# Performance work log

Hardware: AMD Instinct MI355X
Metric: run time of the kernel (lower is better)

Reference implementation:

```python
import jax, jax.numpy as jnp
import numpy as np

LN_EPS = 1e-5  # torch LayerNorm default


def setup_inputs() -> dict:
    key = jax.random.key(0)
    k1, k2, k3 = jax.random.split(key, 3)
    B, L, D = 8, 2048, 1024
    CS, CD = 8192, 16
    x = jax.random.normal(k1, (B, L, D), dtype=jnp.float32)
    # xavier_uniform for Linear(dim, codebook_dim): bound = sqrt(6/(fan_in+fan_out))
    bound = float(np.sqrt(6.0 / (D + CD)))
    W = jax.random.uniform(k2, (CD, D), dtype=jnp.float32, minval=-bound, maxval=bound)
    codebook = jax.random.normal(k3, (CS, CD), dtype=jnp.float32)
    return {"x": x, "W": W, "codebook": codebook}


def reference(x, W, codebook):
    # random projection: (B,L,D) @ (D,CD) -> (B,L,CD)
    z = jnp.einsum("bld,cd->blc", x, W)
    # LayerNorm over last dim, no affine
    mu = jnp.mean(z, axis=-1, keepdims=True)
    var = jnp.mean(jnp.square(z - mu), axis=-1, keepdims=True)
    z = (z - mu) / jnp.sqrt(var + LN_EPS)
    # squared euclidean distance via matmul decomposition (avoids (B,L,CS,CD) tensor):
    # ||z - c||^2 = ||z||^2 - 2 z.c + ||c||^2 ; argmin is identical to argmin of the norm
    z_sq = jnp.sum(jnp.square(z), axis=-1, keepdims=True)        # (B,L,1)
    c_sq = jnp.sum(jnp.square(codebook), axis=-1)                # (CS,)
    d2 = z_sq - 2.0 * jnp.einsum("blc,kc->blk", z, codebook) + c_sq  # (B,L,CS)
    codes = jnp.argmin(d2, axis=-1)                              # (B,L) int32
    return codes
```

## Files before the change

kernel.cpp:

```cpp
#include <hip/hip_runtime.h>
#include <math.h>

#define D      1024
#define CD     16
#define CS     8192
#define ROWS   16384
#define LN_EPS 1e-5f
#define KCHUNK 512
#define NCHUNK (CS / KCHUNK)
#define CPAD   56

typedef __attribute__((ext_vector_type(8))) short short8;
typedef __attribute__((ext_vector_type(4))) float f32x4;

__device__ inline unsigned short bf16_rne(float v) {
    unsigned u = __float_as_uint(v);
    unsigned r = u + 0x7FFFu + ((u >> 16) & 1u);
    return (unsigned short)(r >> 16);
}
__device__ inline short8 ld8(const unsigned short* p) { return *(const short8*)p; }

__device__ inline void split3(float v, unsigned short& a, unsigned short& b, unsigned short& c) {
    unsigned u = __float_as_uint(v);
    unsigned r = u + 0x7FFFu + ((u >> 16) & 1u);
    a = (unsigned short)(r >> 16);
    float r1 = v - __uint_as_float(r & 0xFFFF0000u);
    unsigned u1 = __float_as_uint(r1);
    unsigned r1b = u1 + 0x7FFFu + ((u1 >> 16) & 1u);
    b = (unsigned short)(r1b >> 16);
    float r2 = r1 - __uint_as_float(r1b & 0xFFFF0000u);
    c = bf16_rne(r2);
}

__global__ __launch_bounds__(256) void pack_all(const float* __restrict__ W,
                                                const float* __restrict__ cb,
                                                unsigned short* __restrict__ wb,
                                                unsigned short* __restrict__ cbp,
                                                float* __restrict__ nhc)
{
    const int t = threadIdx.x;
    if (blockIdx.x < 32) {
        int k = blockIdx.x * 256 + t;
        const float* c = cb + (long)k * CD;
        unsigned short* o = cbp + (long)k * 48;
        float csq = 0.f;
        #pragma unroll
        for (int d = 0; d < 16; ++d) {
            float v = c[d];
            csq = fmaf(v, v, csq);
            unsigned short h0, h1, h2;
            split3(v, h0, h1, h2);
            o[d] = h0; o[16 + d] = h1; o[32 + d] = h2;
        }
        nhc[k] = -0.5f * csq;
    } else {
        int tid = (blockIdx.x - 32) * 256 + t;
        int gk   = tid / 192;
        int rem  = tid % 192;
        int term = rem >> 6;
        int L    = rem & 63;
        int n = L & 15, q = L >> 4;
        const float* src = W + n * D + gk * 32 + q * 8;
        unsigned short* dst = wb + (size_t)tid * 8;
        #pragma unroll
        for (int j = 0; j < 8; ++j) {
            unsigned short h0, h1, h2;
            split3(src[j], h0, h1, h2);
            dst[j] = term == 0 ? h0 : (term == 1 ? h1 : h2);
        }
    }
}

__global__ __launch_bounds__(256, 4) void proj_ln(const float* __restrict__ x,
                                                  const unsigned short* __restrict__ wb,
                                                  unsigned short* __restrict__ zp)
{
    __shared__ float part[3][64][4];
    const int t = threadIdx.x;
    const int L = t & 63;
    const int kq = t >> 6;
    const int rt = blockIdx.x;
    const int n = L & 15, q = L >> 4;

    const float* xrow = x + (size_t)(rt * 16 + n) * D + kq * 256 + q * 8;
    const unsigned short* wbase = wb + (size_t)(kq * 8) * 1536;

    f32x4 acc0 = {0.f, 0.f, 0.f, 0.f};
    f32x4 acc1 = {0.f, 0.f, 0.f, 0.f};
    #pragma unroll
    for (int kk = 0; kk < 8; ++kk) {
        float4 xa = *(const float4*)(xrow + kk * 32);
        float4 xb = *(const float4*)(xrow + kk * 32 + 4);
        const unsigned short* wp = wbase + (size_t)kk * 1536 + L * 8;
        short8 w0 = ld8(wp);
        short8 w1 = ld8(wp + 512);
        short8 w2 = ld8(wp + 1024);
        float vs[8] = {xa.x, xa.y, xa.z, xa.w, xb.x, xb.y, xb.z, xb.w};
        short8 x0, x1, x2;
        #pragma unroll
        for (int j = 0; j < 8; ++j) {
            unsigned short h0, h1, h2;
            split3(vs[j], h0, h1, h2);
            x0[j] = (short)h0; x1[j] = (short)h1; x2[j] = (short)h2;
        }
        acc0 = __builtin_amdgcn_mfma_f32_16x16x32_bf16(x0, w0, acc0, 0, 0, 0);
        acc1 = __builtin_amdgcn_mfma_f32_16x16x32_bf16(x0, w1, acc1, 0, 0, 0);
        acc0 = __builtin_amdgcn_mfma_f32_16x16x32_bf16(x1, w0, acc0, 0, 0, 0);
        acc1 = __builtin_amdgcn_mfma_f32_16x16x32_bf16(x1, w1, acc1, 0, 0, 0);
        acc0 = __builtin_amdgcn_mfma_f32_16x16x32_bf16(x0, w2, acc0, 0, 0, 0);
        acc1 = __builtin_amdgcn_mfma_f32_16x16x32_bf16(x2, w0, acc1, 0, 0, 0);
    }

    if (kq != 0) {
        #pragma unroll
        for (int r = 0; r < 4; ++r) part[kq - 1][L][r] = acc0[r] + acc1[r];
    }
    __syncthreads();
    if (kq == 0) {
        #pragma unroll
        for (int r = 0; r < 4; ++r) {
            float zv = acc0[r] + acc1[r] + part[0][L][r] + part[1][L][r] + part[2][L][r];
            float s = zv;
            for (int m = 1; m < 16; m <<= 1) s += __shfl_xor(s, m, 64);
            float mu = s * (1.f / 16.f);
            float dd = zv - mu;
            float v2 = dd * dd;
            for (int m = 1; m < 16; m <<= 1) v2 += __shfl_xor(v2, m, 64);
            float var = v2 * (1.f / 16.f);
            float zn = dd / sqrtf(var + LN_EPS);
            unsigned short h0, h1, h2;
            split3(zn, h0, h1, h2);
            unsigned short* zr = zp + (size_t)(rt * 16 + q * 4 + r) * 48;
            zr[n] = h0; zr[16 + n] = h1; zr[32 + n] = h2;
        }
    }
}

__global__ __launch_bounds__(256, 2) void dist_argmin(const unsigned short* __restrict__ zp,
                                                      const unsigned short* __restrict__ cbp,
                                                      const float* __restrict__ nhc,
                                                      float* __restrict__ pbest,
                                                      int* __restrict__ pidx)
{
    __shared__ __align__(16) unsigned short cl[KCHUNK * CPAD];
    __shared__ float ql[KCHUNK];
    const int t = threadIdx.x;
    const int kbase = blockIdx.y * KCHUNK;

    {
        const float4* src = (const float4*)(cbp + (size_t)kbase * 48);
        #pragma unroll
        for (int i = 0; i < 12; ++i) {
            int idx = t + i * 256;
            int k = idx / 6, c = idx % 6;
            *(float4*)(cl + (size_t)k * CPAD + c * 8) = src[idx];
        }
        if (t < KCHUNK / 4) ((float4*)ql)[t] = ((const float4*)(nhc + kbase))[t];
    }
    __syncthreads();

    const int L = t & 63;
    const int w = t >> 6;
    const int n = L & 15;
    const int q = L >> 4;

    const int oa2 = (q * 8 + 16) & 31;
    const int oa3 = q < 2 ? 32 + q * 8 : (q - 2) * 8;
    const int ob3 = q < 2 ? q * 8 : 16 + q * 8;

    short8 a1[4], a2[4], a3[4];
    const int rt0 = blockIdx.x * 16 + w * 4;
    #pragma unroll
    for (int j = 0; j < 4; ++j) {
        const unsigned short* zr = zp + (size_t)((rt0 + j) * 16 + n) * 48;
        a1[j] = ld8(zr + q * 8);
        a2[j] = ld8(zr + oa2);
        a3[j] = ld8(zr + oa3);
    }

    float best[4][4];
    int   bi[4][4];
    #pragma unroll
    for (int j = 0; j < 4; ++j)
        #pragma unroll
        for (int r = 0; r < 4; ++r) { best[j][r] = -INFINITY; bi[j][r] = 0; }

    #pragma unroll 2
    for (int tt = 0; tt < KCHUNK / 16; ++tt) {
        const unsigned short* cb_t = cl + (size_t)(tt * 16 + n) * CPAD;
        short8 b1 = ld8(cb_t + q * 8);
        short8 b3 = ld8(cb_t + ob3);
        float bneg = ql[tt * 16 + n];
        f32x4 bias = {bneg, bneg, bneg, bneg};
        int code = kbase + tt * 16 + n;
        f32x4 acc[4];
        #pragma unroll
        for (int j = 0; j < 4; ++j)
            acc[j] = __builtin_amdgcn_mfma_f32_16x16x32_bf16(a1[j], b1, bias, 0, 0, 0);
        #pragma unroll
        for (int j = 0; j < 4; ++j)
            acc[j] = __builtin_amdgcn_mfma_f32_16x16x32_bf16(a2[j], b1, acc[j], 0, 0, 0);
        #pragma unroll
        for (int j = 0; j < 4; ++j)
            acc[j] = __builtin_amdgcn_mfma_f32_16x16x32_bf16(a3[j], b3, acc[j], 0, 0, 0);
        #pragma unroll
        for (int j = 0; j < 4; ++j)
            #pragma unroll
            for (int r = 0; r < 4; ++r)
                if (acc[j][r] > best[j][r]) { best[j][r] = acc[j][r]; bi[j][r] = code; }
    }

    #pragma unroll
    for (int mask = 1; mask < 16; mask <<= 1) {
        #pragma unroll
        for (int j = 0; j < 4; ++j)
            #pragma unroll
            for (int r = 0; r < 4; ++r) {
                float s2 = __shfl_xor(best[j][r], mask, 64);
                int   i2 = __shfl_xor(bi[j][r], mask, 64);
                if (s2 > best[j][r] || (s2 == best[j][r] && i2 < bi[j][r])) {
                    best[j][r] = s2; bi[j][r] = i2;
                }
            }
    }
    if (n == 0) {
        #pragma unroll
        for (int j = 0; j < 4; ++j)
            #pragma unroll
            for (int r = 0; r < 4; ++r) {
                int row = (rt0 + j) * 16 + q * 4 + r;
                pbest[(size_t)row * NCHUNK + blockIdx.y] = best[j][r];
                pidx [(size_t)row * NCHUNK + blockIdx.y] = bi[j][r];
            }
    }
}

__global__ __launch_bounds__(256) void merge_argmin(const float* __restrict__ pbest,
                                                    const int* __restrict__ pidx,
                                                    int* __restrict__ out)
{
    const long row = (long)blockIdx.x * 256 + threadIdx.x;
    float best = -INFINITY;
    int   bi   = 0;
    #pragma unroll
    for (int i = 0; i < NCHUNK; ++i) {
        float s = pbest[row * NCHUNK + i];
        if (s > best) { best = s; bi = pidx[row * NCHUNK + i]; }
    }
    out[row] = bi;
}

extern "C" void kernel_launch(void* const* d_in, const int* in_sizes, int n_in,
                              void* d_out, int out_size, void* d_ws, size_t ws_size,
                              hipStream_t stream)
{
    const float* x  = (const float*)d_in[0];
    const float* W  = (const float*)d_in[1];
    const float* cb = (const float*)d_in[2];
    int* out = (int*)d_out;

    char* ws = (char*)d_ws;
    unsigned short* zp  = (unsigned short*)ws;
    unsigned short* cbp = (unsigned short*)(ws + 0x180000);
    float* nhc  = (float*)(ws + 0x240000);
    unsigned short* wb = (unsigned short*)(ws + 0x248000);
    float* pbest = (float*)(ws + 0x260000);
    int*   pidx  = (int*)  (ws + 0x360000);

    pack_all<<<56, 256, 0, stream>>>(W, cb, wb, cbp, nhc);
    proj_ln <<<ROWS / 16, 256, 0, stream>>>(x, wb, zp);
    dist_argmin<<<dim3(ROWS / 256, NCHUNK), 256, 0, stream>>>(zp, cbp, nhc, pbest, pidx);
    merge_argmin<<<ROWS / 256, 256, 0, stream>>>(pbest, pidx, out);
}
```

Measured before the change: 146.4 us.

## Stream pre-swizzled codebook fragments from global memory instead of staging in LDS

The pack kernel now writes the codebook's bf16 split terms in the exact per-lane MFMA fragment order. The distance kernel can then load each B operand directly from global memory with coalesced 16-byte loads, software-prefetched one tile ahead. This drops the LDS staging buffer and the block barrier, which lets the launch bound rise to 4 blocks per CU. The MFMA chains are also interleaved per row tile to reduce accumulator register pressure, at the cost of relying on L2/L1 for codebook reuse across blocks.

```diff
diff --git a/kernel.cpp b/kernel.cpp
--- a/kernel.cpp
+++ b/kernel.cpp
@@ -8,7 +8,6 @@
 #define LN_EPS 1e-5f
 #define KCHUNK 512
 #define NCHUNK (CS / KCHUNK)
-#define CPAD   56
 
 typedef __attribute__((ext_vector_type(8))) short short8;
 typedef __attribute__((ext_vector_type(4))) float f32x4;
@@ -35,26 +34,39 @@
 __global__ __launch_bounds__(256) void pack_all(const float* __restrict__ W,
                                                 const float* __restrict__ cb,
                                                 unsigned short* __restrict__ wb,
-                                                unsigned short* __restrict__ cbp,
+                                                unsigned short* __restrict__ bstream,
                                                 float* __restrict__ nhc)
 {
     const int t = threadIdx.x;
-    if (blockIdx.x < 32) {
-        int k = blockIdx.x * 256 + t;
+    const int b = blockIdx.x;
+    if (b < 32) {
+        int k = b * 256 + t;
         const float* c = cb + (long)k * CD;
-        unsigned short* o = cbp + (long)k * 48;
         float csq = 0.f;
         #pragma unroll
-        for (int d = 0; d < 16; ++d) {
-            float v = c[d];
-            csq = fmaf(v, v, csq);
-            unsigned short h0, h1, h2;
-            split3(v, h0, h1, h2);
-            o[d] = h0; o[16 + d] = h1; o[32 + d] = h2;
-        }
+        for (int d = 0; d < 16; ++d) csq = fmaf(c[d], c[d], csq);
         nhc[k] = -0.5f * csq;
+    } else if (b < 288) {
+        int gid = (b - 32) * 256 + t;
+        int L = gid & 63;
+        int g = (gid >> 6) & 1;
+        int T = gid >> 7;
+        int n = L & 15, q = L >> 4;
+        int k = T * 16 + n;
+        int o = (g == 0) ? q * 8 : (q < 2 ? q * 8 : 16 + q * 8);
+        int term = o >> 4;
+        int d0 = o & 15;
+        const float* c = cb + (long)k * CD + d0;
+        unsigned short out[8];
+        #pragma unroll
+        for (int j = 0; j < 8; ++j) {
+            unsigned short h0, h1, h2;
+            split3(c[j], h0, h1, h2);
+            out[j] = term == 0 ? h0 : (term == 1 ? h1 : h2);
+        }
+        *(short8*)(bstream + (size_t)gid * 8) = *(short8*)out;
     } else {
-        int tid = (blockIdx.x - 32) * 256 + t;
+        int tid = (b - 288) * 256 + t;
         int gk   = tid / 192;
         int rem  = tid % 192;
         int term = rem >> 6;
@@ -136,37 +148,24 @@
     }
 }
 
-__global__ __launch_bounds__(256, 2) void dist_argmin(const unsigned short* __restrict__ zp,
-                                                      const unsigned short* __restrict__ cbp,
+__global__ __launch_bounds__(256, 4) void dist_argmin(const unsigned short* __restrict__ zp,
+                                                      const unsigned short* __restrict__ bstream,
                                                       const float* __restrict__ nhc,
                                                       float* __restrict__ pbest,
                                                       int* __restrict__ pidx)
 {
-    __shared__ __align__(16) unsigned short cl[KCHUNK * CPAD];
-    __shared__ float ql[KCHUNK];
     const int t = threadIdx.x;
-    const int kbase = blockIdx.y * KCHUNK;
-
-    {
-        const float4* src = (const float4*)(cbp + (size_t)kbase * 48);
-        #pragma unroll
-        for (int i = 0; i < 12; ++i) {
-            int idx = t + i * 256;
-            int k = idx / 6, c = idx % 6;
-            *(float4*)(cl + (size_t)k * CPAD + c * 8) = src[idx];
-        }
-        if (t < KCHUNK / 4) ((float4*)ql)[t] = ((const float4*)(nhc + kbase))[t];
-    }
-    __syncthreads();
-
     const int L = t & 63;
     const int w = t >> 6;
     const int n = L & 15;
     const int q = L >> 4;
+    const int kbase = blockIdx.y * KCHUNK;
+    const int Tbase = kbase >> 4;
+
+    const short8* bs = (const short8*)bstream + (size_t)Tbase * 128 + L;
 
     const int oa2 = (q * 8 + 16) & 31;
     const int oa3 = q < 2 ? 32 + q * 8 : (q - 2) * 8;
-    const int ob3 = q < 2 ? q * 8 : 16 + q * 8;
 
     short8 a1[4], a2[4], a3[4];
     const int rt0 = blockIdx.x * 16 + w * 4;
@@ -185,29 +184,30 @@
         #pragma unroll
         for (int r = 0; r < 4; ++r) { best[j][r] = -INFINITY; bi[j][r] = 0; }
 
-    #pragma unroll 2
+    short8 b1n = bs[0];
+    short8 b3n = bs[64];
+    float  qn  = nhc[kbase + n];
+
     for (int tt = 0; tt < KCHUNK / 16; ++tt) {
-        const unsigned short* cb_t = cl + (size_t)(tt * 16 + n) * CPAD;
-        short8 b1 = ld8(cb_t + q * 8);
-        short8 b3 = ld8(cb_t + ob3);
-        float bneg = ql[tt * 16 + n];
-        f32x4 bias = {bneg, bneg, bneg, bneg};
+        short8 b1 = b1n, b3 = b3n;
+        float qv = qn;
+        if (tt + 1 < KCHUNK / 16) {
+            b1n = bs[(tt + 1) * 128];
+            b3n = bs[(tt + 1) * 128 + 64];
+            qn  = nhc[kbase + (tt + 1) * 16 + n];
+        }
+        f32x4 bias = {qv, qv, qv, qv};
         int code = kbase + tt * 16 + n;
-        f32x4 acc[4];
-        #pragma unroll
-        for (int j = 0; j < 4; ++j)
-            acc[j] = __builtin_amdgcn_mfma_f32_16x16x32_bf16(a1[j], b1, bias, 0, 0, 0);
-        #pragma unroll
-        for (int j = 0; j < 4; ++j)
-            acc[j] = __builtin_amdgcn_mfma_f32_16x16x32_bf16(a2[j], b1, acc[j], 0, 0, 0);
-        #pragma unroll
-        for (int j = 0; j < 4; ++j)
-            acc[j] = __builtin_amdgcn_mfma_f32_16x16x32_bf16(a3[j], b3, acc[j], 0, 0, 0);
-        #pragma unroll
-        for (int j = 0; j < 4; ++j)
+        #pragma unroll
+        for (int j = 0; j < 4; ++j) {
+            f32x4 acc;
+            acc = __builtin_amdgcn_mfma_f32_16x16x32_bf16(a1[j], b1, bias, 0, 0, 0);
+            acc = __builtin_amdgcn_mfma_f32_16x16x32_bf16(a2[j], b1, acc, 0, 0, 0);
+            acc = __builtin_amdgcn_mfma_f32_16x16x32_bf16(a3[j], b3, acc, 0, 0, 0);
             #pragma unroll
             for (int r = 0; r < 4; ++r)
-                if (acc[j][r] > best[j][r]) { best[j][r] = acc[j][r]; bi[j][r] = code; }
+                if (acc[r] > best[j][r]) { best[j][r] = acc[r]; bi[j][r] = code; }
+        }
     }
 
     #pragma unroll
@@ -261,14 +261,14 @@
 
     char* ws = (char*)d_ws;
     unsigned short* zp  = (unsigned short*)ws;
-    unsigned short* cbp = (unsigned short*)(ws + 0x180000);
-    float* nhc  = (float*)(ws + 0x240000);
-    unsigned short* wb = (unsigned short*)(ws + 0x248000);
-    float* pbest = (float*)(ws + 0x260000);
-    int*   pidx  = (int*)  (ws + 0x360000);
-
-    pack_all<<<56, 256, 0, stream>>>(W, cb, wb, cbp, nhc);
+    float* nhc  = (float*)(ws + 0x180000);
+    unsigned short* wb = (unsigned short*)(ws + 0x188000);
+    unsigned short* bstream = (unsigned short*)(ws + 0x1A0000);
+    float* pbest = (float*)(ws + 0x2A0000);
+    int*   pidx  = (int*)  (ws + 0x3A0000);
+
+    pack_all<<<312, 256, 0, stream>>>(W, cb, wb, bstream, nhc);
     proj_ln <<<ROWS / 16, 256, 0, stream>>>(x, wb, zp);
-    dist_argmin<<<dim3(ROWS / 256, NCHUNK), 256, 0, stream>>>(zp, cbp, nhc, pbest, pidx);
+    dist_argmin<<<dim3(ROWS / 256, NCHUNK), 256, 0, stream>>>(zp, bstream, nhc, pbest, pidx);
     merge_argmin<<<ROWS / 256, 256, 0, stream>>>(pbest, pidx, out);
 }
```

New measurement: 140.9 us. 3.8% less time.
